# Optimization experiments

Hardware: AMD Instinct MI355X
Metric: run time of the kernel (lower is better)

The kernel has to match this reference:

```python
import jax, jax.numpy as jnp
import numpy as np

C_IN = 256


def setup_inputs() -> dict:
    key = jax.random.key(0)
    ks = jax.random.split(key, 10)
    B, C, H, W = 1, C_IN, 96, 96
    Cq = C // 8
    s = 0.05
    return {
        "x": jax.random.normal(ks[0], (B, C, H, W), dtype=jnp.float32),
        "Wq": jax.random.normal(ks[1], (Cq, C), dtype=jnp.float32) * s,
        "bq": jax.random.normal(ks[2], (Cq,), dtype=jnp.float32) * s,
        "Wk": jax.random.normal(ks[3], (Cq, C), dtype=jnp.float32) * s,
        "bk": jax.random.normal(ks[4], (Cq,), dtype=jnp.float32) * s,
        "Wv": jax.random.normal(ks[5], (C, C), dtype=jnp.float32) * s,
        "bv": jax.random.normal(ks[6], (C,), dtype=jnp.float32) * s,
        "W6": jax.random.normal(ks[7], (C, C), dtype=jnp.float32) * s,
        "b6": jax.random.normal(ks[8], (C,), dtype=jnp.float32) * s,
        "gamma": jnp.ones((1,), dtype=jnp.float32),
    }


def reference(x, Wq, bq, Wk, bk, Wv, bv, W6, b6, gamma):
    # TRM forward (OFS just wraps it). 1x1 convs expressed as einsums.
    B, C, H, W = x.shape
    N = H * W
    scale = C ** -0.5  # 1 / sqrt(in_dim)
    xf = x.reshape(B, C, N)
    q = jnp.einsum('oc,bcn->bon', Wq, xf) + bq[None, :, None]   # (B, C/8, N)
    k = jnp.einsum('oc,bcn->bon', Wk, xf) + bk[None, :, None]   # (B, C/8, N)
    v = jnp.einsum('oc,bcn->bon', Wv, xf) + bv[None, :, None]   # (B, C,   N)
    # energy[b,n,m] = sum_c q[b,c,n] * k[b,c,m]  -> full spatial attention (B,N,N)
    energy = jnp.einsum('bcn,bcm->bnm', q, k)
    att = jax.nn.softmax(energy, axis=-1)
    # out[b,c,n] = sum_m v[b,c,m] * att[b,n,m]
    out = jnp.einsum('bcm,bnm->bcn', v, att)                    # (B, C, N)
    # torch: out.permute(2,0,1) -> (N,B,C); max/mean over C; sum; mean over B
    out_co = out.max(axis=1) + out.mean(axis=1)                 # (B, N)
    x_co = out_co.mean(axis=0).reshape(B, -1) * scale           # valid because B == 1
    x_co = jax.nn.softmax(x_co, axis=-1).reshape(B, 1, H, W)    # spatial gate
    gated = x * x_co
    y = jnp.einsum('oc,bchw->bohw', W6, gated) + b6[None, :, None, None]
    return gamma * y + x + y
```

## Files before the change

kernel.cpp:

```cpp
#include <hip/hip_runtime.h>

#define N 9216
#define CIN 256
#define DQ 32
#define NT 144
#define LOG2E 1.44269504088896340736f

typedef short short8 __attribute__((ext_vector_type(8)));
typedef float floatx4 __attribute__((ext_vector_type(4)));
typedef unsigned short ushort_t;

__device__ __forceinline__ ushort_t f2bf(float f) {
  union { float f; unsigned u; } a; a.f = f;
  unsigned u = a.u;
  u += 0x7fffu + ((u >> 16) & 1u);
  return (ushort_t)(u >> 16);
}
__device__ __forceinline__ ushort_t f2bf_fast(float f) {
  union { float f; unsigned u; } a; a.f = f;
  return (ushort_t)((a.u + 0x8000u) >> 16);
}
__device__ __forceinline__ float bf2f(ushort_t h) {
  union { unsigned u; float f; } a; a.u = ((unsigned)h) << 16;
  return a.f;
}
__device__ __forceinline__ unsigned pack2(float lo, float hi) {
  return ((unsigned)f2bf_fast(hi) << 16) | (unsigned)f2bf_fast(lo);
}
__device__ __forceinline__ short8 mk_bf16x8(const float* p) {
  float4 f0 = *(const float4*)(p);
  float4 f1 = *(const float4*)(p + 4);
  union { unsigned u[4]; short8 v; } r;
  r.u[0] = pack2(f0.x, f0.y);
  r.u[1] = pack2(f0.z, f0.w);
  r.u[2] = pack2(f1.x, f1.y);
  r.u[3] = pack2(f1.z, f1.w);
  return r.v;
}

__device__ __forceinline__ void barrier_lds_only() {
  asm volatile("s_waitcnt lgkmcnt(0)" ::: "memory");
  __builtin_amdgcn_s_barrier();
  asm volatile("" ::: "memory");
}

#define XBT_STRIDE 264

__device__ __forceinline__ void stage_x_tile(
    const float* __restrict__ x, int n0, int t, ushort_t (*xbT)[XBT_STRIDE])
{
  const int p = t & 31, ng = t >> 5;
  unsigned* base = (unsigned*)&xbT[0][0] + (size_t)(ng * 8) * 132;
#pragma unroll
  for (int cc = 0; cc < 4; ++cc) {
    const int c = cc * 64 + 2 * p;
    const float* r0 = x + (size_t)c * N + n0 + ng * 8;
    const float* r1 = r0 + N;
    float4 a0 = *(const float4*)(r0);
    float4 a1 = *(const float4*)(r0 + 4);
    float4 b0 = *(const float4*)(r1);
    float4 b1 = *(const float4*)(r1 + 4);
    unsigned* d = base + (cc * 32 + p);
    d[0 * 132] = pack2(a0.x, b0.x);
    d[1 * 132] = pack2(a0.y, b0.y);
    d[2 * 132] = pack2(a0.z, b0.z);
    d[3 * 132] = pack2(a0.w, b0.w);
    d[4 * 132] = pack2(a1.x, b1.x);
    d[5 * 132] = pack2(a1.y, b1.y);
    d[6 * 132] = pack2(a1.z, b1.z);
    d[7 * 132] = pack2(a1.w, b1.w);
  }
}

__global__ __launch_bounds__(256) void qkv_mfma(
    const float* __restrict__ x,
    const float* __restrict__ Wq, const float* __restrict__ bq,
    const float* __restrict__ Wk, const float* __restrict__ bk,
    const float* __restrict__ Wv, const float* __restrict__ bv,
    ushort_t* __restrict__ qT, ushort_t* __restrict__ kT,
    ushort_t* __restrict__ vG, float* __restrict__ sumExp)
{
  if (blockIdx.x == 0 && blockIdx.y == 0 && threadIdx.x == 0) *sumExp = 0.f;

  __shared__ ushort_t xbT[64][XBT_STRIDE];
  const int t = threadIdx.x;
  const int n0 = blockIdx.x * 64;
  const int oc = blockIdx.y;
  const int w = t >> 6, lane = t & 63;
  const int quad = lane >> 4, l15 = lane & 15;

  stage_x_tile(x, n0, t, xbT);
  __syncthreads();

  const int obase = oc * 64 + w * 16;
  const int oA = obase + l15;
  const float* Arow;
  if (oc == 0) Arow = (obase < 32) ? (Wq + (size_t)oA * CIN)
                                   : (Wk + (size_t)(oA - 32) * CIN);
  else         Arow = Wv + (size_t)(oA - 64) * CIN;

  floatx4 acc[4];
#pragma unroll
  for (int b2 = 0; b2 < 4; ++b2) acc[b2] = (floatx4){0.f, 0.f, 0.f, 0.f};

#pragma unroll
  for (int ks = 0; ks < 8; ++ks) {
    const short8 af = mk_bf16x8(Arow + ks * 32 + 8 * quad);
#pragma unroll
    for (int b2 = 0; b2 < 4; ++b2) {
      const short8 bf = *(const short8*)&xbT[b2 * 16 + l15][ks * 32 + 8 * quad];
      acc[b2] = __builtin_amdgcn_mfma_f32_16x16x32_bf16(af, bf, acc[b2], 0, 0, 0);
    }
  }

#pragma unroll
  for (int b2 = 0; b2 < 4; ++b2) {
    const int n = n0 + b2 * 16 + l15;
#pragma unroll
    for (int r = 0; r < 4; ++r) {
      const int o = obase + 4 * quad + r;
      const float val = acc[b2][r];
      if (oc == 0) {
        if (o < 32) qT[(size_t)n * DQ + o]        = f2bf((val + bq[o]) * LOG2E);
        else        kT[(size_t)n * DQ + (o - 32)] = f2bf(val + bk[o - 32]);
      } else        vG[(size_t)(o - 64) * N + n]  = f2bf(val + bv[o - 64]);
    }
  }
}

__global__ __launch_bounds__(256, 4) void attn_kernel(
    const ushort_t* __restrict__ qT, const ushort_t* __restrict__ kT,
    const ushort_t* __restrict__ vG,
    ushort_t* __restrict__ Opart, float* __restrict__ lpart,
    int base, int rem)
{
  __shared__ ushort_t Pb[2][64][40];

  const int t = threadIdx.x;
  const int w = t >> 6;
  const int lane = t & 63;
  const int quad = lane >> 4;
  const int l15 = lane & 15;
  const int nt = blockIdx.x;
  const int s  = blockIdx.y;
  const int n0 = nt * 64;
  const int sliceIters = base + (s < rem ? 1 : 0);
  const int it0 = s * base + (s < rem ? s : rem);
  const int mbase = it0 * 32;
  const int cw = w * 64;

  const short8 aq =
      *(const short8*)(qT + (size_t)(n0 + 16 * w + l15) * DQ + 8 * quad);

  floatx4 acc[4][4];
#pragma unroll
  for (int a2 = 0; a2 < 4; ++a2)
#pragma unroll
    for (int b2 = 0; b2 < 4; ++b2)
      acc[a2][b2] = (floatx4){0.f, 0.f, 0.f, 0.f};
  float lsum[4] = {0.f, 0.f, 0.f, 0.f};
  const floatx4 z4 = {0.f, 0.f, 0.f, 0.f};

  const ushort_t* kRow  = kT + (size_t)(mbase + l15) * DQ + 8 * quad;
  const ushort_t* vRow0 = vG + (size_t)(cw +  0 + l15) * N + mbase + 8 * quad;
  const ushort_t* vRow1 = vG + (size_t)(cw + 16 + l15) * N + mbase + 8 * quad;
  const ushort_t* vRow2 = vG + (size_t)(cw + 32 + l15) * N + mbase + 8 * quad;
  const ushort_t* vRow3 = vG + (size_t)(cw + 48 + l15) * N + mbase + 8 * quad;

  for (int it = 0; it < sliceIters; ++it) {
    const short8 kb0 = *(const short8*)(kRow);
    const short8 kb1 = *(const short8*)(kRow + 16 * DQ);
    kRow += 32 * DQ;
    const short8 av0 = *(const short8*)(vRow0);
    const short8 av1 = *(const short8*)(vRow1);
    const short8 av2 = *(const short8*)(vRow2);
    const short8 av3 = *(const short8*)(vRow3);
    vRow0 += 32; vRow1 += 32; vRow2 += 32; vRow3 += 32;

    floatx4 s0 = __builtin_amdgcn_mfma_f32_16x16x32_bf16(aq, kb0, z4, 0, 0, 0);
    floatx4 s1 = __builtin_amdgcn_mfma_f32_16x16x32_bf16(aq, kb1, z4, 0, 0, 0);

    ushort_t* pb = &Pb[it & 1][0][0];
#pragma unroll
    for (int r = 0; r < 4; ++r) {
      float p0 = exp2f(s0[r]);
      float p1 = exp2f(s1[r]);
      lsum[r] += p0 + p1;
      const int row = 16 * w + 4 * quad + r;
      pb[row * 40 + l15]      = f2bf_fast(p0);
      pb[row * 40 + 16 + l15] = f2bf_fast(p1);
    }

    barrier_lds_only();

    __builtin_amdgcn_s_setprio(1);
#pragma unroll
    for (int b2 = 0; b2 < 4; ++b2) {
      const short8 pf = *(const short8*)&Pb[it & 1][b2 * 16 + l15][8 * quad];
      acc[0][b2] = __builtin_amdgcn_mfma_f32_16x16x32_bf16(av0, pf, acc[0][b2], 0, 0, 0);
      acc[1][b2] = __builtin_amdgcn_mfma_f32_16x16x32_bf16(av1, pf, acc[1][b2], 0, 0, 0);
      acc[2][b2] = __builtin_amdgcn_mfma_f32_16x16x32_bf16(av2, pf, acc[2][b2], 0, 0, 0);
      acc[3][b2] = __builtin_amdgcn_mfma_f32_16x16x32_bf16(av3, pf, acc[3][b2], 0, 0, 0);
    }
    __builtin_amdgcn_s_setprio(0);
  }

#pragma unroll
  for (int r = 0; r < 4; ++r) {
    float v = lsum[r];
    v += __shfl_xor(v, 1);
    v += __shfl_xor(v, 2);
    v += __shfl_xor(v, 4);
    v += __shfl_xor(v, 8);
    lsum[r] = v;
  }
  if (l15 == 0) {
#pragma unroll
    for (int r = 0; r < 4; ++r)
      lpart[(size_t)s * N + n0 + 16 * w + 4 * quad + r] = lsum[r];
  }

  const size_t basep = ((size_t)s * NT + nt) * 256;
#pragma unroll
  for (int a2 = 0; a2 < 4; ++a2)
#pragma unroll
    for (int b2 = 0; b2 < 4; ++b2)
#pragma unroll
      for (int r = 0; r < 4; ++r) {
        const int c  = cw + a2 * 16 + 4 * quad + r;
        const int nl = b2 * 16 + l15;
        Opart[(basep + c) * 64 + nl] = f2bf(acc[a2][b2][r]);
      }
}

template<int NSL>
__global__ __launch_bounds__(1024) void cco_kernel(
    const ushort_t* __restrict__ Opart, const float* __restrict__ lpart,
    float* __restrict__ e_buf, float* __restrict__ sumExp)
{
  const int nt = blockIdx.x;
  const int t = threadIdx.x;
  const int n = t & 63, ci = t >> 6;
  float mx = -3.4e38f, sm = 0.f;
#pragma unroll
  for (int k = 0; k < 16; ++k) {
    const int c = ci * 16 + k;
    float val = 0.f;
#pragma unroll
    for (int s2 = 0; s2 < NSL; ++s2)
      val += bf2f(Opart[(((size_t)s2 * NT + nt) * 256 + c) * 64 + n]);
    mx = fmaxf(mx, val);
    sm += val;
  }
  __shared__ float rmx[16][64], rsm[16][64];
  rmx[ci][n] = mx; rsm[ci][n] = sm;
  __syncthreads();
  if (t < 64) {
    float m = rmx[0][t], s = rsm[0][t];
#pragma unroll
    for (int g = 1; g < 16; ++g) { m = fmaxf(m, rmx[g][t]); s += rsm[g][t]; }
    float l = 0.f;
#pragma unroll
    for (int s3 = 0; s3 < NSL; ++s3) l += lpart[(size_t)s3 * N + nt * 64 + t];
    const float oc = (m + s * (1.0f / 256.0f)) / l;
    const float ev = exp2f(oc * (0.0625f * LOG2E));
    e_buf[nt * 64 + t] = ev;
    float vs = ev;
    vs += __shfl_xor(vs, 1);  vs += __shfl_xor(vs, 2);
    vs += __shfl_xor(vs, 4);  vs += __shfl_xor(vs, 8);
    vs += __shfl_xor(vs, 16); vs += __shfl_xor(vs, 32);
    if (t == 0) atomicAdd(sumExp, vs);
  }
}

__global__ __launch_bounds__(256) void final_mfma(
    const float* __restrict__ x, const float* __restrict__ W6,
    const float* __restrict__ b6, const float* __restrict__ gamma,
    const float* __restrict__ e_buf, const float* __restrict__ sumExp,
    float* __restrict__ out)
{
  __shared__ ushort_t xbT[64][XBT_STRIDE];
  const int t = threadIdx.x;
  const int n0 = blockIdx.x * 64;
  const int w = t >> 6, lane = t & 63;
  const int quad = lane >> 4, l15 = lane & 15;

  stage_x_tile(x, n0, t, xbT);
  __syncthreads();

  const int obase = blockIdx.y * 64 + w * 16;
  const float* Arow = W6 + (size_t)(obase + l15) * CIN;

  floatx4 acc[4];
#pragma unroll
  for (int b2 = 0; b2 < 4; ++b2) acc[b2] = (floatx4){0.f, 0.f, 0.f, 0.f};

#pragma unroll
  for (int ks = 0; ks < 8; ++ks) {
    const short8 af = mk_bf16x8(Arow + ks * 32 + 8 * quad);
#pragma unroll
    for (int b2 = 0; b2 < 4; ++b2) {
      const short8 bf = *(const short8*)&xbT[b2 * 16 + l15][ks * 32 + 8 * quad];
      acc[b2] = __builtin_amdgcn_mfma_f32_16x16x32_bf16(af, bf, acc[b2], 0, 0, 0);
    }
  }

  const float g1 = 1.0f + gamma[0];
  const float inv = 1.0f / sumExp[0];
#pragma unroll
  for (int b2 = 0; b2 < 4; ++b2) {
    const int n = n0 + b2 * 16 + l15;
    const float xc = e_buf[n] * inv;
#pragma unroll
    for (int r = 0; r < 4; ++r) {
      const int o = obase + 4 * quad + r;
      const float xv = x[(size_t)o * N + n];
      out[(size_t)o * N + n] = xv + g1 * (xc * acc[b2][r] + b6[o]);
    }
  }
}

extern "C" void kernel_launch(void* const* d_in, const int* in_sizes, int n_in,
                              void* d_out, int out_size, void* d_ws, size_t ws_size,
                              hipStream_t stream)
{
  const float* x     = (const float*)d_in[0];
  const float* Wq    = (const float*)d_in[1];
  const float* bq    = (const float*)d_in[2];
  const float* Wk    = (const float*)d_in[3];
  const float* bk    = (const float*)d_in[4];
  const float* Wv    = (const float*)d_in[5];
  const float* bv    = (const float*)d_in[6];
  const float* W6    = (const float*)d_in[7];
  const float* b6    = (const float*)d_in[8];
  const float* gamma = (const float*)d_in[9];
  float* out = (float*)d_out;

  const size_t fixed = (size_t)N * DQ * 2 * 2
                     + (size_t)CIN * N * 2
                     + (size_t)N * 4
                     + 256;
  int nsl = 7;
  size_t need = fixed + (size_t)nsl * NT * 256 * 64 * 2 + (size_t)nsl * N * 4;
  if (ws_size < need) nsl = 4;
  const int totIters = N / 32;
  const int base = totIters / nsl;
  const int rem  = totIters % nsl;

  char* ws = (char*)d_ws;
  const size_t OFF_QT = 0;
  const size_t OFF_KT = OFF_QT + (size_t)N * DQ * 2;
  const size_t OFF_V  = OFF_KT + (size_t)N * DQ * 2;
  const size_t OFF_OP = OFF_V  + (size_t)CIN * N * 2;
  const size_t OFF_LP = OFF_OP + (size_t)nsl * NT * 256 * 64 * 2;
  const size_t OFF_EB = OFF_LP + (size_t)nsl * N * 4;
  const size_t OFF_SE = OFF_EB + (size_t)N * 4;

  ushort_t* qT     = (ushort_t*)(ws + OFF_QT);
  ushort_t* kT     = (ushort_t*)(ws + OFF_KT);
  ushort_t* vG     = (ushort_t*)(ws + OFF_V);
  ushort_t* Opart  = (ushort_t*)(ws + OFF_OP);
  float*    lpart  = (float*)(ws + OFF_LP);
  float*    e_buf  = (float*)(ws + OFF_EB);
  float*    sumExp = (float*)(ws + OFF_SE);

  qkv_mfma<<<dim3(NT, 5), 256, 0, stream>>>(x, Wq, bq, Wk, bk, Wv, bv, qT, kT, vG, sumExp);
  attn_kernel<<<dim3(NT, nsl), 256, 0, stream>>>(qT, kT, vG, Opart, lpart, base, rem);
  if (nsl == 7) cco_kernel<7><<<NT, 1024, 0, stream>>>(Opart, lpart, e_buf, sumExp);
  else          cco_kernel<4><<<NT, 1024, 0, stream>>>(Opart, lpart, e_buf, sumExp);
  final_mfma<<<dim3(NT, 4), 256, 0, stream>>>(x, W6, b6, gamma, e_buf, sumExp, out);
}
```

Baseline: 214.4 us.

## Pre-convert weights to bf16 once and loop output channels per block to reuse staged x

Adds a small kernel that converts Wq, Wk, Wv and W6 to bf16 in workspace, so the GEMM kernels load packed bf16 A-fragments instead of converting fp32 per block. The qkv and final kernels now loop over all output-channel chunks inside one block, so the x tile is staged into LDS once per spatial tile instead of five or four times. The cost is one extra launch and far fewer blocks (144 instead of 720/576), which lowers parallelism and latency hiding on a large GPU.

New measurement: 228.8 us. 6.7% more time.

```diff
diff --git a/kernel.cpp b/kernel.cpp
--- a/kernel.cpp
+++ b/kernel.cpp
@@ -26,16 +26,6 @@
 }
 __device__ __forceinline__ unsigned pack2(float lo, float hi) {
   return ((unsigned)f2bf_fast(hi) << 16) | (unsigned)f2bf_fast(lo);
-}
-__device__ __forceinline__ short8 mk_bf16x8(const float* p) {
-  float4 f0 = *(const float4*)(p);
-  float4 f1 = *(const float4*)(p + 4);
-  union { unsigned u[4]; short8 v; } r;
-  r.u[0] = pack2(f0.x, f0.y);
-  r.u[1] = pack2(f0.z, f0.w);
-  r.u[2] = pack2(f1.x, f1.y);
-  r.u[3] = pack2(f1.z, f1.w);
-  return r.v;
 }
 
 __device__ __forceinline__ void barrier_lds_only() {
@@ -72,58 +62,80 @@
   }
 }
 
+__global__ __launch_bounds__(256) void wconv_kernel(
+    const float* __restrict__ Wq, const float* __restrict__ Wk,
+    const float* __restrict__ Wv, const float* __restrict__ W6,
+    ushort_t* __restrict__ Wb)
+{
+  const int idx = blockIdx.x * 256 + threadIdx.x;
+  const int base = idx * 4;
+  float4 f;
+  if      (base <  8192) f = *(const float4*)(Wq + base);
+  else if (base < 16384) f = *(const float4*)(Wk + base - 8192);
+  else if (base < 81920) f = *(const float4*)(Wv + base - 16384);
+  else                   f = *(const float4*)(W6 + base - 81920);
+  uint2 o;
+  o.x = pack2(f.x, f.y);
+  o.y = pack2(f.z, f.w);
+  *(uint2*)(Wb + base) = o;
+}
+
 __global__ __launch_bounds__(256) void qkv_mfma(
-    const float* __restrict__ x,
-    const float* __restrict__ Wq, const float* __restrict__ bq,
-    const float* __restrict__ Wk, const float* __restrict__ bk,
-    const float* __restrict__ Wv, const float* __restrict__ bv,
+    const float* __restrict__ x, const ushort_t* __restrict__ Wb,
+    const float* __restrict__ bq, const float* __restrict__ bk,
+    const float* __restrict__ bv,
     ushort_t* __restrict__ qT, ushort_t* __restrict__ kT,
     ushort_t* __restrict__ vG, float* __restrict__ sumExp)
 {
-  if (blockIdx.x == 0 && blockIdx.y == 0 && threadIdx.x == 0) *sumExp = 0.f;
+  if (blockIdx.x == 0 && threadIdx.x == 0) *sumExp = 0.f;
 
   __shared__ ushort_t xbT[64][XBT_STRIDE];
   const int t = threadIdx.x;
   const int n0 = blockIdx.x * 64;
-  const int oc = blockIdx.y;
   const int w = t >> 6, lane = t & 63;
   const int quad = lane >> 4, l15 = lane & 15;
 
   stage_x_tile(x, n0, t, xbT);
   __syncthreads();
 
-  const int obase = oc * 64 + w * 16;
-  const int oA = obase + l15;
-  const float* Arow;
-  if (oc == 0) Arow = (obase < 32) ? (Wq + (size_t)oA * CIN)
-                                   : (Wk + (size_t)(oA - 32) * CIN);
-  else         Arow = Wv + (size_t)(oA - 64) * CIN;
-
-  floatx4 acc[4];
-#pragma unroll
-  for (int b2 = 0; b2 < 4; ++b2) acc[b2] = (floatx4){0.f, 0.f, 0.f, 0.f};
-
-#pragma unroll
-  for (int ks = 0; ks < 8; ++ks) {
-    const short8 af = mk_bf16x8(Arow + ks * 32 + 8 * quad);
+  const ushort_t* Wqb = Wb;
+  const ushort_t* Wkb = Wb + 8192;
+  const ushort_t* Wvb = Wb + 16384;
+
+#pragma unroll
+  for (int oc = 0; oc < 5; ++oc) {
+    const int obase = oc * 64 + w * 16;
+    const ushort_t* Arow;
+    if (oc == 0) Arow = (w < 2) ? (Wqb + (size_t)(obase + l15) * CIN)
+                                : (Wkb + (size_t)(obase - 32 + l15) * CIN);
+    else         Arow = Wvb + (size_t)(obase - 64 + l15) * CIN;
+
+    floatx4 acc[4];
+#pragma unroll
+    for (int b2 = 0; b2 < 4; ++b2) acc[b2] = (floatx4){0.f, 0.f, 0.f, 0.f};
+
+#pragma unroll
+    for (int ks = 0; ks < 8; ++ks) {
+      const short8 af = *(const short8*)(Arow + ks * 32 + 8 * quad);
+#pragma unroll
+      for (int b2 = 0; b2 < 4; ++b2) {
+        const short8 bf = *(const short8*)&xbT[b2 * 16 + l15][ks * 32 + 8 * quad];
+        acc[b2] = __builtin_amdgcn_mfma_f32_16x16x32_bf16(af, bf, acc[b2], 0, 0, 0);
+      }
+    }
+
 #pragma unroll
     for (int b2 = 0; b2 < 4; ++b2) {
-      const short8 bf = *(const short8*)&xbT[b2 * 16 + l15][ks * 32 + 8 * quad];
-      acc[b2] = __builtin_amdgcn_mfma_f32_16x16x32_bf16(af, bf, acc[b2], 0, 0, 0);
-    }
-  }
-
-#pragma unroll
-  for (int b2 = 0; b2 < 4; ++b2) {
-    const int n = n0 + b2 * 16 + l15;
-#pragma unroll
-    for (int r = 0; r < 4; ++r) {
-      const int o = obase + 4 * quad + r;
-      const float val = acc[b2][r];
-      if (oc == 0) {
-        if (o < 32) qT[(size_t)n * DQ + o]        = f2bf((val + bq[o]) * LOG2E);
-        else        kT[(size_t)n * DQ + (o - 32)] = f2bf(val + bk[o - 32]);
-      } else        vG[(size_t)(o - 64) * N + n]  = f2bf(val + bv[o - 64]);
+      const int n = n0 + b2 * 16 + l15;
+#pragma unroll
+      for (int r = 0; r < 4; ++r) {
+        const int o = obase + 4 * quad + r;
+        const float val = acc[b2][r];
+        if (oc == 0) {
+          if (o < 32) qT[(size_t)n * DQ + o]        = f2bf((val + bq[o]) * LOG2E);
+          else        kT[(size_t)n * DQ + (o - 32)] = f2bf(val + bk[o - 32]);
+        } else        vG[(size_t)(o - 64) * N + n]  = f2bf(val + bv[o - 64]);
+      }
     }
   }
 }
@@ -274,7 +286,7 @@
 }
 
 __global__ __launch_bounds__(256) void final_mfma(
-    const float* __restrict__ x, const float* __restrict__ W6,
+    const float* __restrict__ x, const ushort_t* __restrict__ W6b,
     const float* __restrict__ b6, const float* __restrict__ gamma,
     const float* __restrict__ e_buf, const float* __restrict__ sumExp,
     float* __restrict__ out)
@@ -288,34 +300,38 @@
   stage_x_tile(x, n0, t, xbT);
   __syncthreads();
 
-  const int obase = blockIdx.y * 64 + w * 16;
-  const float* Arow = W6 + (size_t)(obase + l15) * CIN;
-
-  floatx4 acc[4];
-#pragma unroll
-  for (int b2 = 0; b2 < 4; ++b2) acc[b2] = (floatx4){0.f, 0.f, 0.f, 0.f};
-
-#pragma unroll
-  for (int ks = 0; ks < 8; ++ks) {
-    const short8 af = mk_bf16x8(Arow + ks * 32 + 8 * quad);
-#pragma unroll
-    for (int b2 = 0; b2 < 4; ++b2) {
-      const short8 bf = *(const short8*)&xbT[b2 * 16 + l15][ks * 32 + 8 * quad];
-      acc[b2] = __builtin_amdgcn_mfma_f32_16x16x32_bf16(af, bf, acc[b2], 0, 0, 0);
-    }
-  }
-
   const float g1 = 1.0f + gamma[0];
   const float inv = 1.0f / sumExp[0];
-#pragma unroll
-  for (int b2 = 0; b2 < 4; ++b2) {
-    const int n = n0 + b2 * 16 + l15;
-    const float xc = e_buf[n] * inv;
-#pragma unroll
-    for (int r = 0; r < 4; ++r) {
-      const int o = obase + 4 * quad + r;
-      const float xv = x[(size_t)o * N + n];
-      out[(size_t)o * N + n] = xv + g1 * (xc * acc[b2][r] + b6[o]);
+
+#pragma unroll
+  for (int oc = 0; oc < 4; ++oc) {
+    const int obase = oc * 64 + w * 16;
+    const ushort_t* Arow = W6b + (size_t)(obase + l15) * CIN;
+
+    floatx4 acc[4];
+#pragma unroll
+    for (int b2 = 0; b2 < 4; ++b2) acc[b2] = (floatx4){0.f, 0.f, 0.f, 0.f};
+
+#pragma unroll
+    for (int ks = 0; ks < 8; ++ks) {
+      const short8 af = *(const short8*)(Arow + ks * 32 + 8 * quad);
+#pragma unroll
+      for (int b2 = 0; b2 < 4; ++b2) {
+        const short8 bf = *(const short8*)&xbT[b2 * 16 + l15][ks * 32 + 8 * quad];
+        acc[b2] = __builtin_amdgcn_mfma_f32_16x16x32_bf16(af, bf, acc[b2], 0, 0, 0);
+      }
+    }
+
+#pragma unroll
+    for (int b2 = 0; b2 < 4; ++b2) {
+      const int n = n0 + b2 * 16 + l15;
+      const float xc = e_buf[n] * inv;
+#pragma unroll
+      for (int r = 0; r < 4; ++r) {
+        const int o = obase + 4 * quad + r;
+        const float xv = x[(size_t)o * N + n];
+        out[(size_t)o * N + n] = xv + g1 * (xc * acc[b2][r] + b6[o]);
+      }
     }
   }
 }
@@ -336,7 +352,9 @@
   const float* gamma = (const float*)d_in[9];
   float* out = (float*)d_out;
 
-  const size_t fixed = (size_t)N * DQ * 2 * 2
+  const size_t WB_BYTES = (size_t)(8192 + 8192 + 65536 + 65536) * 2;
+  const size_t fixed = WB_BYTES
+                     + (size_t)N * DQ * 2 * 2
                      + (size_t)CIN * N * 2
                      + (size_t)N * 4
                      + 256;
@@ -348,7 +366,8 @@
   const int rem  = totIters % nsl;
 
   char* ws = (char*)d_ws;
-  const size_t OFF_QT = 0;
+  const size_t OFF_WB = 0;
+  const size_t OFF_QT = OFF_WB + WB_BYTES;
   const size_t OFF_KT = OFF_QT + (size_t)N * DQ * 2;
   const size_t OFF_V  = OFF_KT + (size_t)N * DQ * 2;
   const size_t OFF_OP = OFF_V  + (size_t)CIN * N * 2;
@@ -356,6 +375,7 @@
   const size_t OFF_EB = OFF_LP + (size_t)nsl * N * 4;
   const size_t OFF_SE = OFF_EB + (size_t)N * 4;
 
+  ushort_t* Wb     = (ushort_t*)(ws + OFF_WB);
   ushort_t* qT     = (ushort_t*)(ws + OFF_QT);
   ushort_t* kT     = (ushort_t*)(ws + OFF_KT);
   ushort_t* vG     = (ushort_t*)(ws + OFF_V);
@@ -364,9 +384,10 @@
   float*    e_buf  = (float*)(ws + OFF_EB);
   float*    sumExp = (float*)(ws + OFF_SE);
 
-  qkv_mfma<<<dim3(NT, 5), 256, 0, stream>>>(x, Wq, bq, Wk, bk, Wv, bv, qT, kT, vG, sumExp);
+  wconv_kernel<<<144, 256, 0, stream>>>(Wq, Wk, Wv, W6, Wb);
+  qkv_mfma<<<NT, 256, 0, stream>>>(x, Wb, bq, bk, bv, qT, kT, vG, sumExp);
   attn_kernel<<<dim3(NT, nsl), 256, 0, stream>>>(qT, kT, vG, Opart, lpart, base, rem);
   if (nsl == 7) cco_kernel<7><<<NT, 1024, 0, stream>>>(Opart, lpart, e_buf, sumExp);
   else          cco_kernel<4><<<NT, 1024, 0, stream>>>(Opart, lpart, e_buf, sumExp);
-  final_mfma<<<dim3(NT, 4), 256, 0, stream>>>(x, W6, b6, gamma, e_buf, sumExp, out);
-}
+  final_mfma<<<NT, 256, 0, stream>>>(x, Wb + 81920, b6, gamma, e_buf, sumExp, out);
+}
```
